# Performance work log

Measured on AMD Instinct MI355X. Metric: run time of the kernel, lower is better.

Reference implementation:

```python
import jax, jax.numpy as jnp
import numpy as np
from jax import lax

VOCAB, EMB, HID = 50257, 256, 256
B, T = 64, 2048

def setup_inputs() -> dict:
    key = jax.random.key(0)
    ks = jax.random.split(key, 6)
    s = 1.0 / np.sqrt(HID)
    return {
        "sequence": jax.random.randint(ks[0], (B, T), 0, VOCAB),
        "embedding": jax.random.normal(ks[1], (VOCAB, EMB), jnp.float32),
        "w_ih": jax.random.uniform(ks[2], (3 * HID, EMB), jnp.float32, -s, s),
        "w_hh": jax.random.uniform(ks[3], (3 * HID, HID), jnp.float32, -s, s),
        "b_ih": jax.random.uniform(ks[4], (3 * HID,), jnp.float32, -s, s),
        "b_hh": jax.random.uniform(ks[5], (3 * HID,), jnp.float32, -s, s),
    }

def reference(sequence, embedding, w_ih, w_hh, b_ih, b_hh):
    # sequence: [B,T] int tokens. Original loops per-timestep; math == one GRU pass.
    H = w_hh.shape[1]
    x = embedding[sequence]                       # [B,T,E]
    x = jnp.transpose(x, (1, 0, 2))               # [T,B,E] (time-major)
    # input-side gate pre-activations for all steps at once: [T,B,3H]
    gi = jnp.einsum('tbe,ge->tbg', x, w_ih) + b_ih

    def step(h, gi_t):
        gh = h @ w_hh.T + b_hh                    # [B,3H]
        i_r, i_z, i_n = jnp.split(gi_t, 3, axis=-1)
        h_r, h_z, h_n = jnp.split(gh, 3, axis=-1)
        r = jax.nn.sigmoid(i_r + h_r)
        z = jax.nn.sigmoid(i_z + h_z)
        n = jnp.tanh(i_n + r * h_n)
        h_new = (1.0 - z) * n + z * h
        return h_new, None

    h0 = jnp.zeros((sequence.shape[0], H), dtype=embedding.dtype)
    hT, _ = lax.scan(step, h0, gi)
    return hT[None]                                # [1,B,H] like torch GRU hidden
```

## Files before the change

### kernel.cpp

```cpp
#include <hip/hip_runtime.h>
#include <hip/hip_fp16.h>

#define TSEQ   2048
#define NB     64
#define NE     256
#define NH     256
#define NG     768
#define TCH    64
#define NCHUNK (TSEQ / TCH)

using half2_t = __attribute__((ext_vector_type(2))) _Float16;
typedef unsigned int u32x4 __attribute__((ext_vector_type(4)));
union U4 { u32x4 q; half2_t h[4]; };

__device__ __forceinline__ float dot2f(half2_t a, half2_t b, float c) {
#if __has_builtin(__builtin_amdgcn_fdot2)
  return __builtin_amdgcn_fdot2(a, b, c, false);
#else
  return c + (float)a[0] * (float)b[0] + (float)a[1] * (float)b[1];
#endif
}

__device__ __forceinline__ float fast_exp2(float x) {
#if __has_builtin(__builtin_amdgcn_exp2f)
  return __builtin_amdgcn_exp2f(x);
#else
  return exp2f(x);
#endif
}
__device__ __forceinline__ float fast_rcp(float x) {
#if __has_builtin(__builtin_amdgcn_rcpf)
  return __builtin_amdgcn_rcpf(x);
#else
  return 1.f / x;
#endif
}
__device__ __forceinline__ float sigm(float x) {
  return fast_rcp(1.f + fast_exp2(x * -1.44269504f));
}
__device__ __forceinline__ float tanh_fast(float x) {
  x = fminf(x, 15.f);
  float e = fast_exp2(x * 2.88539008f);
  return (e - 1.f) * fast_rcp(e + 1.f);
}

__global__ void prep_whh(const float* __restrict__ whh, unsigned int* __restrict__ w16) {
  int idx = blockIdx.x * 256 + threadIdx.x;
  if (idx >= 128 * NG) return;
  int row = idx % NG;
  int k2  = idx / NG;
  half2_t p;
  p[0] = (_Float16)whh[row * NH + 2 * k2];
  p[1] = (_Float16)whh[row * NH + 2 * k2 + 1];
  union { half2_t h; unsigned int u; } cvt;
  cvt.h = p;
  w16[(((k2 >> 2) * NG + row) << 2) | (k2 & 3)] = cvt.u;
}

__global__ __launch_bounds__(512) __attribute__((amdgpu_waves_per_eu(2, 2)))
void fused_kernel(const int* __restrict__ seq, const float* __restrict__ emb,
                  const float* __restrict__ wih, const float* __restrict__ bih,
                  const float* __restrict__ bhh, const unsigned int* __restrict__ w16,
                  const float* __restrict__ rec_gi, float* __restrict__ gi_dst,
                  int gi_t0, float* __restrict__ h_state, float* __restrict__ out,
                  int rec_count, int chunk)
{
  __shared__ __align__(16) _Float16 h16[2][NH];
  __shared__ __align__(16) float    xs[64][68];
  __shared__ __align__(16) float    wsh[256][68];
  __shared__ int tok[64];

  const int tid = threadIdx.x;

  if ((int)blockIdx.x < rec_count) {
    const int b    = blockIdx.x;
    const int lane = tid & 63;
    const int wv   = tid >> 6;
    const int jj   = lane & 31;
    const int s    = lane >> 5;
    const int j    = wv * 32 + jj;

    u32x4 wr[16], wz[16], wn[16];
#pragma unroll
    for (int i = 0; i < 16; ++i) {
      const int k2b = s * 16 + i;
      const unsigned int* base = w16 + (((size_t)k2b * NG) << 2);
      wr[i] = *(const u32x4*)(base + ((size_t)j << 2));
      wz[i] = *(const u32x4*)(base + ((size_t)(NH + j) << 2));
      wn[i] = *(const u32x4*)(base + ((size_t)(2 * NH + j) << 2));
    }
#pragma unroll
    for (int i = 0; i < 16; ++i) {
      asm volatile("" : "+v"(wr[i]), "+v"(wz[i]), "+v"(wn[i]));
    }

    const float bn = bhh[2 * NH + j];
    float hreg = 0.f;
    if (chunk != 0) hreg = h_state[b * NH + j];
    if (s == 0) h16[0][j] = (_Float16)hreg;
    __syncthreads();

    const float* gbase = rec_gi + (size_t)b * NG;
    float gr = gbase[j], gz = gbase[NH + j], gn = gbase[2 * NH + j];

#pragma unroll 1
    for (int t = 0; t < TCH; ++t) {
      const int tn = (t + 1) & (TCH - 1);
      const float* gt = gbase + (size_t)tn * NB * NG;
      float grn = gt[j], gzn = gt[NH + j], gnn = gt[2 * NH + j];

      float ar = 0.f, az = 0.f, an = 0.f;
      const char* hb = (const char*)h16 + ((t & 1) << 9) + (s << 8);
#pragma unroll
      for (int i = 0; i < 16; ++i) {
        U4 hu; hu.q = *(const u32x4*)(hb + (i << 4));
        U4 ru; ru.q = wr[i];
        U4 zu; zu.q = wz[i];
        U4 nu; nu.q = wn[i];
#pragma unroll
        for (int q = 0; q < 4; ++q) {
          ar = dot2f(hu.h[q], ru.h[q], ar);
          az = dot2f(hu.h[q], zu.h[q], az);
          an = dot2f(hu.h[q], nu.h[q], an);
        }
      }
      ar += __shfl_xor(ar, 32, 64);
      az += __shfl_xor(az, 32, 64);
      an += __shfl_xor(an, 32, 64);

      const float r = sigm(gr + ar);
      const float z = sigm(gz + az);
      const float n = tanh_fast(gn + r * (an + bn));
      hreg = n + z * (hreg - n);

      if (s == 0) h16[(t + 1) & 1][j] = (_Float16)hreg;
      gr = grn; gz = gzn; gn = gnn;
      __syncthreads();
    }
    if (s == 0) {
      h_state[b * NH + j] = hreg;
      if (out) out[b * NH + j] = hreg;
    }
  } else {
    if (gi_dst == nullptr) return;
    const int gb   = blockIdx.x - rec_count;
    const int tl   = gb & 63;
    const int greg = gb >> 6;
    const int g0   = greg * 256;
    const int t    = gi_t0 + tl;
    if (tid < 64) tok[tid] = seq[tid * TSEQ + t];
    const int tx = tid & 31;
    const int ty = tid >> 5;
    float acc[4][8];
#pragma unroll
    for (int i = 0; i < 4; ++i)
#pragma unroll
      for (int c8 = 0; c8 < 8; ++c8) acc[i][c8] = 0.f;

    for (int kb = 0; kb < 4; ++kb) {
      __syncthreads();
#pragma unroll
      for (int it = 0; it < 2; ++it) {
        int i = it * 512 + tid;
        int r = i >> 4, c = i & 15;
        *(float4*)(&xs[r][c * 4]) =
            *(const float4*)(emb + (size_t)tok[r] * NE + kb * 64 + c * 4);
      }
#pragma unroll
      for (int it = 0; it < 8; ++it) {
        int i = it * 512 + tid;
        int r = i >> 4, c = i & 15;
        *(float4*)(&wsh[r][c * 4]) =
            *(const float4*)(wih + (size_t)(g0 + r) * NE + kb * 64 + c * 4);
      }
      __syncthreads();
#pragma unroll 4
      for (int k4 = 0; k4 < 16; ++k4) {
        float4 xf[4], wf[8];
#pragma unroll
        for (int i = 0; i < 4; ++i) xf[i] = *(const float4*)(&xs[ty * 4 + i][k4 * 4]);
#pragma unroll
        for (int c8 = 0; c8 < 8; ++c8) wf[c8] = *(const float4*)(&wsh[tx + 32 * c8][k4 * 4]);
#pragma unroll
        for (int i = 0; i < 4; ++i)
#pragma unroll
          for (int c8 = 0; c8 < 8; ++c8)
            acc[i][c8] += xf[i].x * wf[c8].x + xf[i].y * wf[c8].y +
                          xf[i].z * wf[c8].z + xf[i].w * wf[c8].w;
      }
    }
#pragma unroll
    for (int i = 0; i < 4; ++i) {
      const int brow = ty * 4 + i;
      float* dst = gi_dst + ((size_t)(tl * NB + brow)) * NG + g0;
#pragma unroll
      for (int c8 = 0; c8 < 8; ++c8) {
        const int col = tx + 32 * c8;
        const int g = g0 + col;
        float bias = bih[g] + (g < 2 * NH ? bhh[g] : 0.f);
        dst[col] = acc[i][c8] + bias;
      }
    }
  }
}

extern "C" void kernel_launch(void* const* d_in, const int* in_sizes, int n_in,
                              void* d_out, int out_size, void* d_ws, size_t ws_size,
                              hipStream_t stream) {
  (void)in_sizes; (void)n_in; (void)out_size; (void)ws_size;
  const int*   seq = (const int*)d_in[0];
  const float* emb = (const float*)d_in[1];
  const float* wih = (const float*)d_in[2];
  const float* whh = (const float*)d_in[3];
  const float* bih = (const float*)d_in[4];
  const float* bhh = (const float*)d_in[5];
  float* out = (float*)d_out;
  char*  ws  = (char*)d_ws;

  unsigned int* w16     = (unsigned int*)(ws);
  float*        h_state = (float*)(ws + 393216);
  float*        gi0     = (float*)(ws + 458752);
  float*        gi1     = (float*)(ws + 458752 + 12582912);

  prep_whh<<<dim3(384), dim3(256), 0, stream>>>(whh, w16);

  fused_kernel<<<dim3(192), dim3(512), 0, stream>>>(
      seq, emb, wih, bih, bhh, w16,
      nullptr, gi0, 0, h_state, nullptr, 0, 0);

  for (int c = 0; c < NCHUNK; ++c) {
    float* rd  = (c & 1) ? gi1 : gi0;
    float* wr_ = (c & 1) ? gi0 : gi1;
    const bool last = (c == NCHUNK - 1);
    const int grid  = last ? NB : NB + 192;
    fused_kernel<<<dim3(grid), dim3(512), 0, stream>>>(
        seq, emb, wih, bih, bhh, w16,
        rd, last ? nullptr : wr_, (c + 1) * TCH, h_state,
        last ? out : nullptr, NB, c);
  }
}
```

Measured before the change: 2.430 ms.

## Split GRU recurrence K-dimension four ways across 1024-thread blocks

The block size doubles to 1024 threads. The recurrent dot product is now split across four lane groups of 16, so each thread holds half as many W_hh registers, and the partial sums are combined with two cross-lane shuffles. The hidden-state buffer in shared memory is padded to avoid bank conflicts. The gi prefetch register pipeline is dropped in favour of direct loads each step, and the input-projection branch is re-tiled for the larger block. This aims to shorten the serial per-step latency with more parallelism, at the cost of extra shuffles, a wider barrier and unhidden global loads of gi.

```diff
diff --git a/kernel.cpp b/kernel.cpp
--- a/kernel.cpp
+++ b/kernel.cpp
@@ -57,7 +57,7 @@
   w16[(((k2 >> 2) * NG + row) << 2) | (k2 & 3)] = cvt.u;
 }
 
-__global__ __launch_bounds__(512) __attribute__((amdgpu_waves_per_eu(2, 2)))
+__global__ __launch_bounds__(1024)
 void fused_kernel(const int* __restrict__ seq, const float* __restrict__ emb,
                   const float* __restrict__ wih, const float* __restrict__ bih,
                   const float* __restrict__ bhh, const unsigned int* __restrict__ w16,
@@ -65,7 +65,7 @@
                   int gi_t0, float* __restrict__ h_state, float* __restrict__ out,
                   int rec_count, int chunk)
 {
-  __shared__ __align__(16) _Float16 h16[2][NH];
+  __shared__ __align__(16) _Float16 h16[2][4][72];
   __shared__ __align__(16) float    xs[64][68];
   __shared__ __align__(16) float    wsh[256][68];
   __shared__ int tok[64];
@@ -76,43 +76,39 @@
     const int b    = blockIdx.x;
     const int lane = tid & 63;
     const int wv   = tid >> 6;
-    const int jj   = lane & 31;
-    const int s    = lane >> 5;
-    const int j    = wv * 32 + jj;
-
-    u32x4 wr[16], wz[16], wn[16];
-#pragma unroll
-    for (int i = 0; i < 16; ++i) {
-      const int k2b = s * 16 + i;
+    const int j    = wv * 16 + (lane & 15);
+    const int s    = lane >> 4;
+
+    u32x4 wr[8], wz[8], wn[8];
+#pragma unroll
+    for (int i = 0; i < 8; ++i) {
+      const int k2b = s * 8 + i;
       const unsigned int* base = w16 + (((size_t)k2b * NG) << 2);
       wr[i] = *(const u32x4*)(base + ((size_t)j << 2));
       wz[i] = *(const u32x4*)(base + ((size_t)(NH + j) << 2));
       wn[i] = *(const u32x4*)(base + ((size_t)(2 * NH + j) << 2));
     }
 #pragma unroll
-    for (int i = 0; i < 16; ++i) {
+    for (int i = 0; i < 8; ++i) {
       asm volatile("" : "+v"(wr[i]), "+v"(wz[i]), "+v"(wn[i]));
     }
 
     const float bn = bhh[2 * NH + j];
     float hreg = 0.f;
     if (chunk != 0) hreg = h_state[b * NH + j];
-    if (s == 0) h16[0][j] = (_Float16)hreg;
+    if (s == 0) h16[0][j >> 6][j & 63] = (_Float16)hreg;
     __syncthreads();
 
-    const float* gbase = rec_gi + (size_t)b * NG;
-    float gr = gbase[j], gz = gbase[NH + j], gn = gbase[2 * NH + j];
+    const float* gpj = rec_gi + (size_t)b * NG + j;
 
 #pragma unroll 1
     for (int t = 0; t < TCH; ++t) {
-      const int tn = (t + 1) & (TCH - 1);
-      const float* gt = gbase + (size_t)tn * NB * NG;
-      float grn = gt[j], gzn = gt[NH + j], gnn = gt[2 * NH + j];
+      const float gr = gpj[0], gz = gpj[NH], gn = gpj[2 * NH];
 
       float ar = 0.f, az = 0.f, an = 0.f;
-      const char* hb = (const char*)h16 + ((t & 1) << 9) + (s << 8);
-#pragma unroll
-      for (int i = 0; i < 16; ++i) {
+      const char* hb = (const char*)&h16[t & 1][s][0];
+#pragma unroll
+      for (int i = 0; i < 8; ++i) {
         U4 hu; hu.q = *(const u32x4*)(hb + (i << 4));
         U4 ru; ru.q = wr[i];
         U4 zu; zu.q = wz[i];
@@ -124,17 +120,17 @@
           an = dot2f(hu.h[q], nu.h[q], an);
         }
       }
-      ar += __shfl_xor(ar, 32, 64);
-      az += __shfl_xor(az, 32, 64);
-      an += __shfl_xor(an, 32, 64);
+      ar += __shfl_xor(ar, 16, 64);  ar += __shfl_xor(ar, 32, 64);
+      az += __shfl_xor(az, 16, 64);  az += __shfl_xor(az, 32, 64);
+      an += __shfl_xor(an, 16, 64);  an += __shfl_xor(an, 32, 64);
 
       const float r = sigm(gr + ar);
       const float z = sigm(gz + az);
       const float n = tanh_fast(gn + r * (an + bn));
       hreg = n + z * (hreg - n);
 
-      if (s == 0) h16[(t + 1) & 1][j] = (_Float16)hreg;
-      gr = grn; gz = gzn; gn = gnn;
+      if (s == 0) h16[(t + 1) & 1][j >> 6][j & 63] = (_Float16)hreg;
+      gpj += NB * NG;
       __syncthreads();
     }
     if (s == 0) {
@@ -143,32 +139,29 @@
     }
   } else {
     if (gi_dst == nullptr) return;
-    const int gb   = blockIdx.x - rec_count;
-    const int tl   = gb & 63;
-    const int greg = gb >> 6;
-    const int g0   = greg * 256;
-    const int t    = gi_t0 + tl;
+    const int gb = blockIdx.x - rec_count;
+    const int tl = gb & 63;
+    const int g0 = (gb >> 6) * 256;
+    const int t  = gi_t0 + tl;
     if (tid < 64) tok[tid] = seq[tid * TSEQ + t];
     const int tx = tid & 31;
     const int ty = tid >> 5;
-    float acc[4][8];
-#pragma unroll
-    for (int i = 0; i < 4; ++i)
+    float acc[2][8];
+#pragma unroll
+    for (int i = 0; i < 2; ++i)
 #pragma unroll
       for (int c8 = 0; c8 < 8; ++c8) acc[i][c8] = 0.f;
 
     for (int kb = 0; kb < 4; ++kb) {
       __syncthreads();
-#pragma unroll
-      for (int it = 0; it < 2; ++it) {
-        int i = it * 512 + tid;
-        int r = i >> 4, c = i & 15;
+      {
+        int r = tid >> 4, c = tid & 15;
         *(float4*)(&xs[r][c * 4]) =
             *(const float4*)(emb + (size_t)tok[r] * NE + kb * 64 + c * 4);
       }
 #pragma unroll
-      for (int it = 0; it < 8; ++it) {
-        int i = it * 512 + tid;
+      for (int it = 0; it < 4; ++it) {
+        int i = it * 1024 + tid;
         int r = i >> 4, c = i & 15;
         *(float4*)(&wsh[r][c * 4]) =
             *(const float4*)(wih + (size_t)(g0 + r) * NE + kb * 64 + c * 4);
@@ -176,13 +169,13 @@
       __syncthreads();
 #pragma unroll 4
       for (int k4 = 0; k4 < 16; ++k4) {
-        float4 xf[4], wf[8];
-#pragma unroll
-        for (int i = 0; i < 4; ++i) xf[i] = *(const float4*)(&xs[ty * 4 + i][k4 * 4]);
+        float4 xf[2], wf[8];
+#pragma unroll
+        for (int i = 0; i < 2; ++i) xf[i] = *(const float4*)(&xs[ty * 2 + i][k4 * 4]);
 #pragma unroll
         for (int c8 = 0; c8 < 8; ++c8) wf[c8] = *(const float4*)(&wsh[tx + 32 * c8][k4 * 4]);
 #pragma unroll
-        for (int i = 0; i < 4; ++i)
+        for (int i = 0; i < 2; ++i)
 #pragma unroll
           for (int c8 = 0; c8 < 8; ++c8)
             acc[i][c8] += xf[i].x * wf[c8].x + xf[i].y * wf[c8].y +
@@ -190,8 +183,8 @@
       }
     }
 #pragma unroll
-    for (int i = 0; i < 4; ++i) {
-      const int brow = ty * 4 + i;
+    for (int i = 0; i < 2; ++i) {
+      const int brow = ty * 2 + i;
       float* dst = gi_dst + ((size_t)(tl * NB + brow)) * NG + g0;
 #pragma unroll
       for (int c8 = 0; c8 < 8; ++c8) {
@@ -224,7 +217,7 @@
 
   prep_whh<<<dim3(384), dim3(256), 0, stream>>>(whh, w16);
 
-  fused_kernel<<<dim3(192), dim3(512), 0, stream>>>(
+  fused_kernel<<<dim3(192), dim3(1024), 0, stream>>>(
       seq, emb, wih, bih, bhh, w16,
       nullptr, gi0, 0, h_state, nullptr, 0, 0);
 
@@ -233,7 +226,7 @@
     float* wr_ = (c & 1) ? gi0 : gi1;
     const bool last = (c == NCHUNK - 1);
     const int grid  = last ? NB : NB + 192;
-    fused_kernel<<<dim3(grid), dim3(512), 0, stream>>>(
+    fused_kernel<<<dim3(grid), dim3(1024), 0, stream>>>(
         seq, emb, wih, bih, bhh, w16,
         rd, last ? nullptr : wr_, (c + 1) * TCH, h_state,
         last ? out : nullptr, NB, c);
```

Measured after the change: 2.657 ms. 1.09x slower.

## Hand-write recurrent GRU step loop in inline assembly with pinned register weights

Applied to the files above, without the earlier changes.

Replaces the compiler-generated recurrent loop with an inline-asm loop. The hidden-weight fragments are pinned in fixed VGPRs v64-v255, and the loop is unrolled by two over the ping-pong h buffer. LDS reads are software-pipelined, the split-K halves are combined with ds_bpermute instead of a shuffle, and the gate math uses raw exp/rcp instructions. The w_hh prep layout is changed to match per-thread contiguous loads, and shared memory becomes a single pool. It aims to cut the per-timestep latency of the serial dependency chain. In exchange it brings heavy register clobbering, manual waitcnt correctness, and the removal of the waves_per_eu attribute.

```diff
diff --git a/kernel.cpp b/kernel.cpp
--- a/kernel.cpp
+++ b/kernel.cpp
@@ -8,56 +8,141 @@
 #define NG     768
 #define TCH    64
 #define NCHUNK (TSEQ / TCH)
-
-using half2_t = __attribute__((ext_vector_type(2))) _Float16;
-typedef unsigned int u32x4 __attribute__((ext_vector_type(4)));
-union U4 { u32x4 q; half2_t h[4]; };
-
-__device__ __forceinline__ float dot2f(half2_t a, half2_t b, float c) {
-#if __has_builtin(__builtin_amdgcn_fdot2)
-  return __builtin_amdgcn_fdot2(a, b, c, false);
-#else
-  return c + (float)a[0] * (float)b[0] + (float)a[1] * (float)b[1];
-#endif
-}
-
-__device__ __forceinline__ float fast_exp2(float x) {
-#if __has_builtin(__builtin_amdgcn_exp2f)
-  return __builtin_amdgcn_exp2f(x);
-#else
-  return exp2f(x);
-#endif
-}
-__device__ __forceinline__ float fast_rcp(float x) {
-#if __has_builtin(__builtin_amdgcn_rcpf)
-  return __builtin_amdgcn_rcpf(x);
-#else
-  return 1.f / x;
-#endif
-}
-__device__ __forceinline__ float sigm(float x) {
-  return fast_rcp(1.f + fast_exp2(x * -1.44269504f));
-}
-__device__ __forceinline__ float tanh_fast(float x) {
-  x = fminf(x, 15.f);
-  float e = fast_exp2(x * 2.88539008f);
-  return (e - 1.f) * fast_rcp(e + 1.f);
-}
+#define POOL_BYTES 87552
 
 __global__ void prep_whh(const float* __restrict__ whh, unsigned int* __restrict__ w16) {
   int idx = blockIdx.x * 256 + threadIdx.x;
-  if (idx >= 128 * NG) return;
-  int row = idx % NG;
-  int k2  = idx / NG;
-  half2_t p;
-  p[0] = (_Float16)whh[row * NH + 2 * k2];
-  p[1] = (_Float16)whh[row * NH + 2 * k2 + 1];
-  union { half2_t h; unsigned int u; } cvt;
-  cvt.h = p;
-  w16[(((k2 >> 2) * NG + row) << 2) | (k2 & 3)] = cvt.u;
+  if (idx >= 98304) return;
+  int c  = idx & 3;
+  int i  = (idx >> 2) & 15;
+  int g  = (idx >> 6) % 3;
+  int js = idx / 192;
+  int s  = js & 1;
+  int j  = js >> 1;
+  int k  = s * 128 + i * 8 + 2 * c;
+  const float* src = whh + (size_t)(g * 256 + j) * 256 + k;
+  union { struct { _Float16 a, b; } h; unsigned int u; } cvt;
+  cvt.h.a = (_Float16)src[0];
+  cvt.h.b = (_Float16)src[1];
+  w16[idx] = cvt.u;
 }
 
-__global__ __launch_bounds__(512) __attribute__((amdgpu_waves_per_eu(2, 2)))
+#define DOT12(H0,H1,H2,H3,R0,R1,R2,R3,Z0,Z1,Z2,Z3,N0,N1,N2,N3) \
+  "v_dot2_f32_f16 v16, v" H0 ", v" R0 ", v16\n\t" \
+  "v_dot2_f32_f16 v17, v" H0 ", v" Z0 ", v17\n\t" \
+  "v_dot2_f32_f16 v18, v" H0 ", v" N0 ", v18\n\t" \
+  "v_dot2_f32_f16 v16, v" H1 ", v" R1 ", v16\n\t" \
+  "v_dot2_f32_f16 v17, v" H1 ", v" Z1 ", v17\n\t" \
+  "v_dot2_f32_f16 v18, v" H1 ", v" N1 ", v18\n\t" \
+  "v_dot2_f32_f16 v16, v" H2 ", v" R2 ", v16\n\t" \
+  "v_dot2_f32_f16 v17, v" H2 ", v" Z2 ", v17\n\t" \
+  "v_dot2_f32_f16 v18, v" H2 ", v" N2 ", v18\n\t" \
+  "v_dot2_f32_f16 v16, v" H3 ", v" R3 ", v16\n\t" \
+  "v_dot2_f32_f16 v17, v" H3 ", v" Z3 ", v17\n\t" \
+  "v_dot2_f32_f16 v18, v" H3 ", v" N3 ", v18\n\t"
+
+#define RSTEP(O0,O1,O2,O3,O4,O5,O6,O7,O8,O9,O10,O11,O12,O13,O14,O15) \
+  "global_load_dword v12, v3, %[gip]\n\t" \
+  "global_load_dword v13, v3, %[gip] offset:1024\n\t" \
+  "global_load_dword v14, v3, %[gip] offset:2048\n\t" \
+  "v_add_u32 v3, 0x30000, v3\n\t" \
+  "v_mov_b32 v16, 0\n\t" \
+  "v_mov_b32 v17, 0\n\t" \
+  "v_mov_b32 v18, 0\n\t" \
+  "ds_read_b128 v[4:7], v2 offset:" O0 "\n\t" \
+  "ds_read_b128 v[8:11], v2 offset:" O1 "\n\t" \
+  "s_waitcnt lgkmcnt(1)\n\t" \
+  DOT12("4","5","6","7",  "64","65","66","67",    "128","129","130","131","192","193","194","195") \
+  "ds_read_b128 v[4:7], v2 offset:" O2 "\n\t" \
+  "s_waitcnt lgkmcnt(1)\n\t" \
+  DOT12("8","9","10","11","68","69","70","71",    "132","133","134","135","196","197","198","199") \
+  "ds_read_b128 v[8:11], v2 offset:" O3 "\n\t" \
+  "s_waitcnt lgkmcnt(1)\n\t" \
+  DOT12("4","5","6","7",  "72","73","74","75",    "136","137","138","139","200","201","202","203") \
+  "ds_read_b128 v[4:7], v2 offset:" O4 "\n\t" \
+  "s_waitcnt lgkmcnt(1)\n\t" \
+  DOT12("8","9","10","11","76","77","78","79",    "140","141","142","143","204","205","206","207") \
+  "ds_read_b128 v[8:11], v2 offset:" O5 "\n\t" \
+  "s_waitcnt lgkmcnt(1)\n\t" \
+  DOT12("4","5","6","7",  "80","81","82","83",    "144","145","146","147","208","209","210","211") \
+  "ds_read_b128 v[4:7], v2 offset:" O6 "\n\t" \
+  "s_waitcnt lgkmcnt(1)\n\t" \
+  DOT12("8","9","10","11","84","85","86","87",    "148","149","150","151","212","213","214","215") \
+  "ds_read_b128 v[8:11], v2 offset:" O7 "\n\t" \
+  "s_waitcnt lgkmcnt(1)\n\t" \
+  DOT12("4","5","6","7",  "88","89","90","91",    "152","153","154","155","216","217","218","219") \
+  "ds_read_b128 v[4:7], v2 offset:" O8 "\n\t" \
+  "s_waitcnt lgkmcnt(1)\n\t" \
+  DOT12("8","9","10","11","92","93","94","95",    "156","157","158","159","220","221","222","223") \
+  "ds_read_b128 v[8:11], v2 offset:" O9 "\n\t" \
+  "s_waitcnt lgkmcnt(1)\n\t" \
+  DOT12("4","5","6","7",  "96","97","98","99",    "160","161","162","163","224","225","226","227") \
+  "ds_read_b128 v[4:7], v2 offset:" O10 "\n\t" \
+  "s_waitcnt lgkmcnt(1)\n\t" \
+  DOT12("8","9","10","11","100","101","102","103","164","165","166","167","228","229","230","231") \
+  "ds_read_b128 v[8:11], v2 offset:" O11 "\n\t" \
+  "s_waitcnt lgkmcnt(1)\n\t" \
+  DOT12("4","5","6","7",  "104","105","106","107","168","169","170","171","232","233","234","235") \
+  "ds_read_b128 v[4:7], v2 offset:" O12 "\n\t" \
+  "s_waitcnt lgkmcnt(1)\n\t" \
+  DOT12("8","9","10","11","108","109","110","111","172","173","174","175","236","237","238","239") \
+  "ds_read_b128 v[8:11], v2 offset:" O13 "\n\t" \
+  "s_waitcnt lgkmcnt(1)\n\t" \
+  DOT12("4","5","6","7",  "112","113","114","115","176","177","178","179","240","241","242","243") \
+  "ds_read_b128 v[4:7], v2 offset:" O14 "\n\t" \
+  "s_waitcnt lgkmcnt(1)\n\t" \
+  DOT12("8","9","10","11","116","117","118","119","180","181","182","183","244","245","246","247") \
+  "ds_read_b128 v[8:11], v2 offset:" O15 "\n\t" \
+  "s_waitcnt lgkmcnt(1)\n\t" \
+  DOT12("4","5","6","7",  "120","121","122","123","184","185","186","187","248","249","250","251") \
+  "s_waitcnt lgkmcnt(0)\n\t" \
+  DOT12("8","9","10","11","124","125","126","127","188","189","190","191","252","253","254","255")
+
+#define REC_TAIL(WOF) \
+  "ds_bpermute_b32 v20, v19, v16\n\t" \
+  "ds_bpermute_b32 v21, v19, v17\n\t" \
+  "ds_bpermute_b32 v22, v19, v18\n\t" \
+  "s_waitcnt lgkmcnt(0)\n\t" \
+  "v_add_f32 v16, v16, v20\n\t" \
+  "v_add_f32 v17, v17, v21\n\t" \
+  "v_add_f32 v18, v18, v22\n\t" \
+  "s_waitcnt vmcnt(0)\n\t" \
+  "v_add_f32 v20, v12, v16\n\t" \
+  "v_mul_f32 v20, 0xbfb8aa3b, v20\n\t" \
+  "v_exp_f32 v20, v20\n\t" \
+  "s_nop 0\n\t" \
+  "v_add_f32 v20, 1.0, v20\n\t" \
+  "v_rcp_f32 v20, v20\n\t" \
+  "s_nop 0\n\t" \
+  "v_add_f32 v21, v13, v17\n\t" \
+  "v_mul_f32 v21, 0xbfb8aa3b, v21\n\t" \
+  "v_exp_f32 v21, v21\n\t" \
+  "s_nop 0\n\t" \
+  "v_add_f32 v21, 1.0, v21\n\t" \
+  "v_rcp_f32 v21, v21\n\t" \
+  "s_nop 0\n\t" \
+  "v_add_f32 v22, v18, v28\n\t" \
+  "v_fma_f32 v22, v20, v22, v14\n\t" \
+  "v_min_f32 v22, 0x41700000, v22\n\t" \
+  "v_mul_f32 v22, 0x4038aa3b, v22\n\t" \
+  "v_exp_f32 v22, v22\n\t" \
+  "s_nop 0\n\t" \
+  "v_add_f32 v23, -1.0, v22\n\t" \
+  "v_add_f32 v22, 1.0, v22\n\t" \
+  "v_rcp_f32 v22, v22\n\t" \
+  "s_nop 0\n\t" \
+  "v_mul_f32 v22, v23, v22\n\t" \
+  "v_sub_f32 v23, v24, v22\n\t" \
+  "v_fma_f32 v24, v21, v23, v22\n\t" \
+  "v_cvt_f16_f32 v25, v24\n\t" \
+  "ds_write_b16 v29, v25 offset:" WOF "\n\t" \
+  "s_waitcnt lgkmcnt(0)\n\t" \
+  "s_barrier\n\t"
+
+#define WLD(D0,D1,OFF) \
+  "global_load_dwordx4 v[" D0 ":" D1 "], %[wof], %[wptr] offset:" OFF "\n\t"
+
+__global__ __launch_bounds__(512)
 void fused_kernel(const int* __restrict__ seq, const float* __restrict__ emb,
                   const float* __restrict__ wih, const float* __restrict__ bih,
                   const float* __restrict__ bhh, const unsigned int* __restrict__ w16,
@@ -65,89 +150,100 @@
                   int gi_t0, float* __restrict__ h_state, float* __restrict__ out,
                   int rec_count, int chunk)
 {
-  __shared__ __align__(16) _Float16 h16[2][NH];
-  __shared__ __align__(16) float    xs[64][68];
-  __shared__ __align__(16) float    wsh[256][68];
-  __shared__ int tok[64];
-
+  __shared__ __align__(16) char smem[POOL_BYTES];
   const int tid = threadIdx.x;
 
   if ((int)blockIdx.x < rec_count) {
-    const int b    = blockIdx.x;
-    const int lane = tid & 63;
-    const int wv   = tid >> 6;
-    const int jj   = lane & 31;
-    const int s    = lane >> 5;
-    const int j    = wv * 32 + jj;
-
-    u32x4 wr[16], wz[16], wn[16];
-#pragma unroll
-    for (int i = 0; i < 16; ++i) {
-      const int k2b = s * 16 + i;
-      const unsigned int* base = w16 + (((size_t)k2b * NG) << 2);
-      wr[i] = *(const u32x4*)(base + ((size_t)j << 2));
-      wz[i] = *(const u32x4*)(base + ((size_t)(NH + j) << 2));
-      wn[i] = *(const u32x4*)(base + ((size_t)(2 * NH + j) << 2));
-    }
-#pragma unroll
-    for (int i = 0; i < 16; ++i) {
-      asm volatile("" : "+v"(wr[i]), "+v"(wz[i]), "+v"(wn[i]));
-    }
-
-    const float bn = bhh[2 * NH + j];
-    float hreg = 0.f;
-    if (chunk != 0) hreg = h_state[b * NH + j];
-    if (s == 0) h16[0][j] = (_Float16)hreg;
+    const int b = blockIdx.x;
+    const unsigned lane = tid & 63;
+    const unsigned jj   = (unsigned)(tid >> 6) * 32 + (lane & 31);
+    const unsigned sh   = lane >> 5;
+
+    float h0 = 0.f;
+    if (chunk != 0) h0 = h_state[b * NH + jj];
+    const float bnv = bhh[2 * NH + jj];
+    ((_Float16*)smem)[jj] = (_Float16)h0;
     __syncthreads();
 
-    const float* gbase = rec_gi + (size_t)b * NG;
-    float gr = gbase[j], gz = gbase[NH + j], gn = gbase[2 * NH + j];
-
-#pragma unroll 1
-    for (int t = 0; t < TCH; ++t) {
-      const int tn = (t + 1) & (TCH - 1);
-      const float* gt = gbase + (size_t)tn * NB * NG;
-      float grn = gt[j], gzn = gt[NH + j], gnn = gt[2 * NH + j];
-
-      float ar = 0.f, az = 0.f, an = 0.f;
-      const char* hb = (const char*)h16 + ((t & 1) << 9) + (s << 8);
-#pragma unroll
-      for (int i = 0; i < 16; ++i) {
-        U4 hu; hu.q = *(const u32x4*)(hb + (i << 4));
-        U4 ru; ru.q = wr[i];
-        U4 zu; zu.q = wz[i];
-        U4 nu; nu.q = wn[i];
-#pragma unroll
-        for (int q = 0; q < 4; ++q) {
-          ar = dot2f(hu.h[q], ru.h[q], ar);
-          az = dot2f(hu.h[q], zu.h[q], az);
-          an = dot2f(hu.h[q], nu.h[q], an);
-        }
-      }
-      ar += __shfl_xor(ar, 32, 64);
-      az += __shfl_xor(az, 32, 64);
-      an += __shfl_xor(an, 32, 64);
-
-      const float r = sigm(gr + ar);
-      const float z = sigm(gz + az);
-      const float n = tanh_fast(gn + r * (an + bn));
-      hreg = n + z * (hreg - n);
-
-      if (s == 0) h16[(t + 1) & 1][j] = (_Float16)hreg;
-      gr = grn; gz = gzn; gn = gnn;
-      __syncthreads();
-    }
-    if (s == 0) {
-      h_state[b * NH + j] = hreg;
-      if (out) out[b * NH + j] = hreg;
-    }
+    const unsigned pool0 = (unsigned)(uintptr_t)(smem);
+    const unsigned hrd = pool0 + sh * 256;
+    const unsigned hwa = pool0 + jj * 2;
+    const unsigned gio = jj * 4;
+    const unsigned bpa = (lane ^ 32u) << 2;
+    const unsigned wof = (jj * 2 + sh) * 768;
+    const float* gib = rec_gi + (size_t)b * NG;
+
+    float hout;
+    asm volatile(
+      "v_mov_b32 v2, %[hrd]\n\t"
+      "v_mov_b32 v3, %[gio]\n\t"
+      "v_mov_b32 v19, %[bpa]\n\t"
+      "v_mov_b32 v24, %[h0]\n\t"
+      "v_mov_b32 v28, %[bn]\n\t"
+      "v_mov_b32 v29, %[hwa]\n\t"
+      WLD("64","67","0")    WLD("68","71","16")   WLD("72","75","32")   WLD("76","79","48")
+      WLD("80","83","64")   WLD("84","87","80")   WLD("88","91","96")   WLD("92","95","112")
+      WLD("96","99","128")  WLD("100","103","144")WLD("104","107","160")WLD("108","111","176")
+      WLD("112","115","192")WLD("116","119","208")WLD("120","123","224")WLD("124","127","240")
+      WLD("128","131","256")WLD("132","135","272")WLD("136","139","288")WLD("140","143","304")
+      WLD("144","147","320")WLD("148","151","336")WLD("152","155","352")WLD("156","159","368")
+      WLD("160","163","384")WLD("164","167","400")WLD("168","171","416")WLD("172","175","432")
+      WLD("176","179","448")WLD("180","183","464")WLD("184","187","480")WLD("188","191","496")
+      WLD("192","195","512")WLD("196","199","528")WLD("200","203","544")WLD("204","207","560")
+      WLD("208","211","576")WLD("212","215","592")WLD("216","219","608")WLD("220","223","624")
+      WLD("224","227","640")WLD("228","231","656")WLD("232","235","672")WLD("236","239","688")
+      WLD("240","243","704")WLD("244","247","720")WLD("248","251","736")WLD("252","255","752")
+      "s_waitcnt vmcnt(0)\n\t"
+      "s_mov_b32 s20, 32\n\t"
+      "1:\n\t"
+      RSTEP("0","16","32","48","64","80","96","112",
+            "128","144","160","176","192","208","224","240")
+      REC_TAIL("512")
+      RSTEP("512","528","544","560","576","592","608","624",
+            "640","656","672","688","704","720","736","752")
+      REC_TAIL("0")
+      "s_sub_u32 s20, s20, 1\n\t"
+      "s_cmp_lg_u32 s20, 0\n\t"
+      "s_cbranch_scc1 1b\n\t"
+      "v_mov_b32 %[hout], v24\n\t"
+      : [hout] "=v"(hout)
+      : [hrd] "v"(hrd), [gio] "v"(gio), [bpa] "v"(bpa), [h0] "v"(h0),
+        [bn] "v"(bnv), [hwa] "v"(hwa), [wof] "v"(wof),
+        [wptr] "s"(w16), [gip] "s"(gib)
+      : "memory","scc","s20",
+        "v2","v3","v4","v5","v6","v7","v8","v9","v10","v11","v12","v13","v14",
+        "v16","v17","v18","v19","v20","v21","v22","v23","v24","v25","v28","v29",
+        "v64","v65","v66","v67","v68","v69","v70","v71","v72","v73","v74","v75",
+        "v76","v77","v78","v79","v80","v81","v82","v83","v84","v85","v86","v87",
+        "v88","v89","v90","v91","v92","v93","v94","v95","v96","v97","v98","v99",
+        "v100","v101","v102","v103","v104","v105","v106","v107","v108","v109",
+        "v110","v111","v112","v113","v114","v115","v116","v117","v118","v119",
+        "v120","v121","v122","v123","v124","v125","v126","v127","v128","v129",
+        "v130","v131","v132","v133","v134","v135","v136","v137","v138","v139",
+        "v140","v141","v142","v143","v144","v145","v146","v147","v148","v149",
+        "v150","v151","v152","v153","v154","v155","v156","v157","v158","v159",
+        "v160","v161","v162","v163","v164","v165","v166","v167","v168","v169",
+        "v170","v171","v172","v173","v174","v175","v176","v177","v178","v179",
+        "v180","v181","v182","v183","v184","v185","v186","v187","v188","v189",
+        "v190","v191","v192","v193","v194","v195","v196","v197","v198","v199",
+        "v200","v201","v202","v203","v204","v205","v206","v207","v208","v209",
+        "v210","v211","v212","v213","v214","v215","v216","v217","v218","v219",
+        "v220","v221","v222","v223","v224","v225","v226","v227","v228","v229",
+        "v230","v231","v232","v233","v234","v235","v236","v237","v238","v239",
+        "v240","v241","v242","v243","v244","v245","v246","v247","v248","v249",
+        "v250","v251","v252","v253","v254","v255");
+
+    h_state[b * NH + jj] = hout;
+    if (out) out[b * NH + jj] = hout;
   } else {
     if (gi_dst == nullptr) return;
-    const int gb   = blockIdx.x - rec_count;
-    const int tl   = gb & 63;
-    const int greg = gb >> 6;
-    const int g0   = greg * 256;
-    const int t    = gi_t0 + tl;
+    float (*xs)[68]  = (float(*)[68])smem;
+    float (*wsh)[68] = (float(*)[68])(smem + 17408);
+    int*  tok        = (int*)(smem + 17408 + 69632);
+    const int gb = blockIdx.x - rec_count;
+    const int tl = gb & 63;
+    const int g0 = (gb >> 6) * 256;
+    const int t  = gi_t0 + tl;
     if (tid < 64) tok[tid] = seq[tid * TSEQ + t];
     const int tx = tid & 31;
     const int ty = tid >> 5;
```

Measured after the change: 2.599 ms. 7.0% more time.
